# Optimization experiments

Hardware: AMD Instinct MI355X
Metric: run time of the kernel (lower is better)

## Reference

```python
import jax, jax.numpy as jnp
import numpy as np

B, N, DIM, HEADS, DEPTH, MLP = 4, 1024, 256, 4, 4, 1024
DH = DIM // HEADS
EPS = 1e-5


def _ln(x, g, b):
    mu = jnp.mean(x, axis=-1, keepdims=True)
    var = jnp.mean((x - mu) ** 2, axis=-1, keepdims=True)
    return (x - mu) / jnp.sqrt(var + EPS) * g + b


def setup_inputs() -> dict:
    key = jax.random.key(0)
    ks = jax.random.split(key, 10)
    s = 0.02
    p = {}
    p["x"] = jax.random.normal(ks[0], (B, N, DIM), jnp.float32)
    p["attn_bias"] = jax.random.normal(ks[1], (2, B, HEADS, N, N), jnp.float32)
    p["ln1_g"] = jnp.ones((DEPTH, DIM), jnp.float32)
    p["ln1_b"] = jnp.zeros((DEPTH, DIM), jnp.float32)
    p["Wkv"] = jax.random.normal(ks[2], (DEPTH, DIM, 2 * DIM), jnp.float32) * s
    p["Wq"] = jax.random.normal(ks[3], (DEPTH, DIM, DIM), jnp.float32) * s
    p["Wo"] = jax.random.normal(ks[4], (DEPTH, DIM, DIM), jnp.float32) * s
    p["bo"] = jnp.zeros((DEPTH, DIM), jnp.float32)
    p["ln2_g"] = jnp.ones((DEPTH, DIM), jnp.float32)
    p["ln2_b"] = jnp.zeros((DEPTH, DIM), jnp.float32)
    p["W1"] = jax.random.normal(ks[5], (DEPTH, DIM, MLP), jnp.float32) * s
    p["b1"] = jnp.zeros((DEPTH, MLP), jnp.float32)
    p["W2"] = jax.random.normal(ks[6], (DEPTH, MLP, DIM), jnp.float32) * s
    p["b2"] = jnp.zeros((DEPTH, DIM), jnp.float32)
    p["Wg"] = jax.random.normal(ks[7], (DIM, DIM), jnp.float32) * s
    p["lng_g"] = jnp.ones((DIM,), jnp.float32)
    p["lng_b"] = jnp.zeros((DIM,), jnp.float32)
    return p


def reference(x, attn_bias, ln1_g, ln1_b, Wkv, Wq, Wo, bo, ln2_g, ln2_b, W1, b1, W2, b2, Wg, lng_g, lng_b):
    scale = DIM ** -0.5
    add_attn = attn_bias[0] + attn_bias[1]            # [B,H,N,N]
    # aggregation bias matrices are layer-invariant (recomputed identically each layer in torch)
    A = jnp.mean(attn_bias[0], axis=1)                # [B,N,N]
    S = jnp.mean(attn_bias[1], axis=1)
    G = jax.nn.softmax(A * S, axis=2)                 # [B,N,N]

    def split_heads(t):  # [B,N,DIM] -> [B,H,N,DH]
        return t.reshape(B, N, HEADS, DH).transpose(0, 2, 1, 3)

    for l in range(DEPTH):
        # softmax-GCN aggregation
        x_ma = jax.nn.relu(_ln(jnp.matmul(G, x) @ Wg, lng_g, lng_b))
        # attention (PreNorm on x only; q comes from un-normed x_ma)
        xn = _ln(x, ln1_g[l], ln1_b[l])
        kv = xn @ Wkv[l]
        k, v = jnp.split(kv, 2, axis=-1)
        q = x_ma @ Wq[l]
        qh, kh, vh = split_heads(q), split_heads(k), split_heads(v)
        dots = jnp.einsum('bhid,bhjd->bhij', qh, kh) * scale + add_attn
        attn = jax.nn.softmax(dots, axis=-1)
        out = jnp.einsum('bhij,bhjd->bhid', attn, vh)
        out = out.transpose(0, 2, 1, 3).reshape(B, N, DIM)
        x = x + out @ Wo[l] + bo[l]
        # feed-forward (exact GELU, matching torch nn.GELU default)
        xn2 = _ln(x, ln2_g[l], ln2_b[l])
        x = x + jax.nn.gelu(xn2 @ W1[l] + b1[l], approximate=False) @ W2[l] + b2[l]
    return x
```

## Files before the change

### kernel.cpp

```cpp
#include <hip/hip_runtime.h>
#include <hip/hip_bf16.h>
#include <math.h>

typedef unsigned short u16;
typedef __bf16 bf16x8 __attribute__((ext_vector_type(8)));
typedef float f32x4 __attribute__((ext_vector_type(4)));
typedef unsigned int u32x4 __attribute__((ext_vector_type(4)));
typedef unsigned short u16x4 __attribute__((ext_vector_type(4)));

#define B_ 4
#define N_ 1024
#define DIM_ 256
#define HEADS_ 4
#define DH_ 64
#define MLP_ 1024
#define DEPTH_ 4

__device__ __forceinline__ float r2f(u16 r){ return __uint_as_float(((unsigned)r)<<16); }
__device__ __forceinline__ u16 f2r(float f){ __hip_bfloat16 h = __float2bfloat16(f); return *(u16*)&h; }

__device__ __forceinline__ float gelu_exact(float v){
  return 0.5f*v*(1.0f + erff(v*0.70710678118654752440f));
}

#define MFMA16(a,b,c) __builtin_amdgcn_mfma_f32_16x16x32_bf16(a,b,c,0,0,0)

__global__ void prep_fused(const float* __restrict__ bias, u16* __restrict__ G, u16* __restrict__ bsum,
                           const float* __restrict__ X, u16* __restrict__ Y,
                           const float* __restrict__ g, const float* __restrict__ bvec){
  if (blockIdx.x < 4096){
    int blk = blockIdx.x;
    int i = blk & (N_-1);
    int b = blk >> 10;
    int t = threadIdx.x;
    __shared__ float red[256];
    long long base0 = ((long long)(b*HEADS_)*N_ + i)*(long long)N_;
    const long long hs = (long long)N_*N_;
    const long long cs = (long long)B_*HEADS_*N_*N_;
    int j0 = t*4;
    f32x4 a = {0.f,0.f,0.f,0.f}, s = {0.f,0.f,0.f,0.f};
    #pragma unroll
    for (int h=0;h<HEADS_;h++){
      f32x4 x0 = __builtin_nontemporal_load((const f32x4*)(bias + base0 + h*hs + j0));
      f32x4 x1 = __builtin_nontemporal_load((const f32x4*)(bias + cs + base0 + h*hs + j0));
      a += x0; s += x1;
      u16x4 pk;
      #pragma unroll
      for (int k=0;k<4;k++) pk[k] = f2r(x0[k]+x1[k]);
      __builtin_nontemporal_store(pk, (u16x4*)(bsum + base0 + h*hs + j0));
    }
    float v[4]; float lmax = -3e38f;
    #pragma unroll
    for (int k=0;k<4;k++){ v[k] = (a[k]*0.25f)*(s[k]*0.25f); lmax = fmaxf(lmax, v[k]); }
    red[t]=lmax; __syncthreads();
    for (int st=128;st>0;st>>=1){ if(t<st) red[t]=fmaxf(red[t],red[t+st]); __syncthreads(); }
    float m = red[0]; __syncthreads();
    float e[4]; float lsum = 0.f;
    #pragma unroll
    for (int k=0;k<4;k++){ e[k] = __expf(v[k]-m); lsum += e[k]; }
    red[t]=lsum; __syncthreads();
    for (int st=128;st>0;st>>=1){ if(t<st) red[t]+=red[t+st]; __syncthreads(); }
    float inv = 1.0f/red[0];
    u16* Grow = G + ((long long)b*N_ + i)*(long long)N_;
    u16x4 pg;
    #pragma unroll
    for (int k=0;k<4;k++) pg[k] = f2r(e[k]*inv);
    *(u16x4*)(Grow + j0) = pg;
  } else {
    int row = (blockIdx.x-4096)*8 + (threadIdx.x>>5);
    int cg = threadIdx.x&31;
    const float* xp = X + (long long)row*DIM_ + cg*8;
    f32x4 v0 = *(const f32x4*)xp;
    f32x4 v1 = *(const f32x4*)(xp+4);
    float s = v0[0]+v0[1]+v0[2]+v0[3]+v1[0]+v1[1]+v1[2]+v1[3];
    s += __shfl_xor(s,1); s += __shfl_xor(s,2); s += __shfl_xor(s,4); s += __shfl_xor(s,8); s += __shfl_xor(s,16);
    float mu = s*(1.0f/256.0f);
    float s2 = 0.f;
    #pragma unroll
    for (int k=0;k<4;k++){ float d=v0[k]-mu; s2 += d*d; }
    #pragma unroll
    for (int k=0;k<4;k++){ float d=v1[k]-mu; s2 += d*d; }
    s2 += __shfl_xor(s2,1); s2 += __shfl_xor(s2,2); s2 += __shfl_xor(s2,4); s2 += __shfl_xor(s2,8); s2 += __shfl_xor(s2,16);
    float rstd = rsqrtf(s2*(1.0f/256.0f)+1e-5f);
    f32x4 g0 = *(const f32x4*)(g + cg*8);
    f32x4 g1 = *(const f32x4*)(g + cg*8 + 4);
    f32x4 b0 = *(const f32x4*)(bvec + cg*8);
    f32x4 b1 = *(const f32x4*)(bvec + cg*8 + 4);
    u16x4 p0, p1;
    #pragma unroll
    for (int k=0;k<4;k++) p0[k] = f2r((v0[k]-mu)*rstd*g0[k] + b0[k]);
    #pragma unroll
    for (int k=0;k<4;k++) p1[k] = f2r((v1[k]-mu)*rstd*g1[k] + b1[k]);
    u16* yp = Y + (long long)row*DIM_ + cg*8;
    *(u16x4*)yp = p0;
    *(u16x4*)(yp+4) = p1;
  }
}

__global__ void tcast_all(const float* __restrict__ Wkv, const float* __restrict__ Wq,
                          const float* __restrict__ Wo, const float* __restrict__ W1,
                          const float* __restrict__ W2, const float* __restrict__ Wg,
                          const float* __restrict__ xin,
                          u16* WkvT, u16* WqT, u16* WoT, u16* W1T, u16* W2T, u16* WgT, u16* xT){
  int z = blockIdx.z;
  const float* I; u16* O; int ldin, R, C;
  if (z < 4)       { I = Wkv + z*131072;      O = WkvT + z*131072;      ldin=512;  R=256;  C=512;  }
  else if (z < 8)  { I = Wq  + (z-4)*65536;   O = WqT  + (z-4)*65536;   ldin=256;  R=256;  C=256;  }
  else if (z < 12) { I = Wo  + (z-8)*65536;   O = WoT  + (z-8)*65536;   ldin=256;  R=256;  C=256;  }
  else if (z < 16) { I = W1  + (z-12)*262144; O = W1T  + (z-12)*262144; ldin=1024; R=256;  C=1024; }
  else if (z < 20) { I = W2  + (z-16)*262144; O = W2T  + (z-16)*262144; ldin=256;  R=1024; C=256;  }
  else if (z == 20){ I = Wg;                  O = WgT;                  ldin=256;  R=256;  C=256;  }
  else             { I = xin + (z-21)*262144; O = xT   + (z-21)*262144; ldin=256;  R=1024; C=256;  }
  int c0 = blockIdx.x*32, r0 = blockIdx.y*32;
  if (c0 >= C || r0 >= R) return;
  __shared__ float tile[32][33];
  int tx = threadIdx.x, ty = threadIdx.y;
  #pragma unroll
  for (int i=0;i<4;i++)
    tile[ty*4+i][tx] = I[(long long)(r0+ty*4+i)*ldin + c0+tx];
  __syncthreads();
  #pragma unroll
  for (int i=0;i<4;i++)
    O[(long long)(c0+ty*4+i)*R + r0+tx] = f2r(tile[tx][ty*4+i]);
}

__global__ __launch_bounds__(512, 2) void layer_pre(
    const u16* __restrict__ Gb, const u16* __restrict__ xT, const u16* __restrict__ xnb,
    const u16* __restrict__ WgT, const u16* __restrict__ WqT, const u16* __restrict__ WkvT,
    const float* __restrict__ lng, const float* __restrict__ lnb,
    u16* __restrict__ qb, u16* __restrict__ kvb, u16* __restrict__ vt)
{
  __shared__ float Gx_s[16][264];
  __shared__ float t2_s[16][264];
  __shared__ u16  xma_s[16][264];
  int tid = threadIdx.x;
  int w = tid>>6, lane = tid&63, lr = lane&15, qd = lane>>4;
  int bid = blockIdx.x;

  if (bid >= 256){
    int row0 = (bid-256)*16;
    int batch = row0>>10;
    const u16* Ap = xnb + (long long)(row0+lr)*DIM_;
    f32x4 acc[4] = {};
    for (int k0=0;k0<256;k0+=32){
      bf16x8 af = *(const bf16x8*)(Ap + k0 + qd*8);
      #pragma unroll
      for (int i=0;i<4;i++){
        bf16x8 bf = *(const bf16x8*)(WkvT + (long long)((w*4+i)*16+lr)*256 + k0 + qd*8);
        acc[i] = MFMA16(af,bf,acc[i]);
      }
    }
    #pragma unroll
    for (int i=0;i<4;i++){
      int col = (w*4+i)*16+lr;
      #pragma unroll
      for (int r=0;r<4;r++){
        int row = row0+qd*4+r;
        float v = acc[i][r];
        kvb[(long long)row*512 + col] = f2r(v);
        if (col >= 256)
          vt[(long long)batch*262144 + (long long)(col-256)*1024 + (row&1023)] = f2r(v);
      }
    }
    return;
  }

  int row0 = bid*16;
  int batch = row0>>10, brow0 = row0&1023;

  {
    int kw = w>>2, cw = w&3;
    const u16* Ap = Gb + (long long)batch*1048576 + (long long)(brow0+lr)*1024 + kw*512;
    const u16* Bp = xT + (long long)batch*262144 + (long long)kw*512;
    f32x4 acc[4] = {};
    for (int k0=0;k0<512;k0+=32){
      bf16x8 af = __builtin_nontemporal_load((const bf16x8*)(Ap + k0 + qd*8));
      #pragma unroll
      for (int nt=0;nt<4;nt++){
        bf16x8 bf = *(const bf16x8*)(Bp + (long long)(cw*64+nt*16+lr)*1024 + k0 + qd*8);
        acc[nt] = MFMA16(af,bf,acc[nt]);
      }
    }
    if (kw==0){
      #pragma unroll
      for (int nt=0;nt<4;nt++)
        #pragma unroll
        for (int r=0;r<4;r++) Gx_s[qd*4+r][cw*64+nt*16+lr] = acc[nt][r];
    }
    __syncthreads();
    if (kw==1){
      #pragma unroll
      for (int nt=0;nt<4;nt++)
        #pragma unroll
        for (int r=0;r<4;r++) Gx_s[qd*4+r][cw*64+nt*16+lr] += acc[nt][r];
    }
    __syncthreads();
  }
  {
    int r = tid>>5, cg2 = tid&31;
    #pragma unroll
    for (int i=0;i<8;i++) xma_s[r][cg2*8+i] = f2r(Gx_s[r][cg2*8+i]);
  }
  __syncthreads();
  {
    f32x4 acc[2] = {};
    for (int k0=0;k0<256;k0+=32){
      bf16x8 af = *(const bf16x8*)&xma_s[lr][k0+qd*8];
      #pragma unroll
      for (int i=0;i<2;i++){
        bf16x8 bf = *(const bf16x8*)(WgT + (long long)((w*2+i)*16+lr)*256 + k0 + qd*8);
        acc[i] = MFMA16(af,bf,acc[i]);
      }
    }
    #pragma unroll
    for (int i=0;i<2;i++)
      #pragma unroll
      for (int r=0;r<4;r++) t2_s[qd*4+r][(w*2+i)*16+lr] = acc[i][r];
  }
  __syncthreads();
  {
    int r = tid>>5, cg2 = tid&31;
    float v[8]; float s=0.f;
    #pragma unroll
    for (int i=0;i<8;i++){ v[i] = t2_s[r][cg2*8+i]; s += v[i]; }
    s += __shfl_xor(s,1); s += __shfl_xor(s,2); s += __shfl_xor(s,4); s += __shfl_xor(s,8); s += __shfl_xor(s,16);
    float mu = s*(1.0f/256.0f);
    float s2=0.f;
    #pragma unroll
    for (int i=0;i<8;i++){ float d=v[i]-mu; s2 += d*d; }
    s2 += __shfl_xor(s2,1); s2 += __shfl_xor(s2,2); s2 += __shfl_xor(s2,4); s2 += __shfl_xor(s2,8); s2 += __shfl_xor(s2,16);
    float rstd = rsqrtf(s2*(1.0f/256.0f)+1e-5f);
    #pragma unroll
    for (int i=0;i<8;i++){
      int c = cg2*8+i;
      float y = (v[i]-mu)*rstd*lng[c] + lnb[c];
      xma_s[r][c] = f2r(fmaxf(y,0.f));
    }
  }
  __syncthreads();
  {
    f32x4 acc[2] = {};
    for (int k0=0;k0<256;k0+=32){
      bf16x8 af = *(const bf16x8*)&xma_s[lr][k0+qd*8];
      #pragma unroll
      for (int i=0;i<2;i++){
        bf16x8 bf = *(const bf16x8*)(WqT + (long long)((w*2+i)*16+lr)*256 + k0 + qd*8);
        acc[i] = MFMA16(af,bf,acc[i]);
      }
    }
    #pragma unroll
    for (int i=0;i<2;i++)
      #pragma unroll
      for (int r=0;r<4;r++)
        qb[(long long)(row0+qd*4+r)*DIM_ + (w*2+i)*16+lr] = f2r(acc[i][r]);
  }
}

#define APSMEM 84224
__global__ __launch_bounds__(1024, 2) void attn_post(
    const u16* __restrict__ qb, const u16* __restrict__ kvb,
    const u16* __restrict__ vt, const u16* __restrict__ bsum,
    const float* __restrict__ resx,
    const u16* __restrict__ WoT, const float* __restrict__ bo,
    const float* __restrict__ ln2g, const float* __restrict__ ln2b,
    const u16* __restrict__ W1T, const float* __restrict__ b1,
    const u16* __restrict__ W2T, const float* __restrict__ b2,
    float* __restrict__ xf_out,
    const float* __restrict__ ln1g_next, const float* __restrict__ ln1b_next,
    u16* __restrict__ xn_out, u16* __restrict__ xT_out)
{
  __shared__ __align__(16) char smem[APSMEM];
  u16 (*sb)[16][72]   = (u16 (*)[16][72])smem;
  u16 (*Pl)[16][72]   = (u16 (*)[16][72])(smem+36864);
  float (*Ml)[16]     = (float(*)[16])(smem+73728);
  float (*Ll)[16]     = (float(*)[16])(smem+74752);
  float (*Ol)[16][68] = (float(*)[16][68])smem;
  u16  (*ao_s)[264]   = (u16 (*)[264])(smem+75776);
  float (*v_s)[264]   = (float(*)[264])smem;
  u16  (*xn2_s)[264]  = (u16 (*)[264])(smem+16896);
  u16  (*h1_s)[1048]  = (u16 (*)[1048])(smem+25344);
  float (*xnew_s)[264]= (float(*)[264])(smem+58880);

  int tid = threadIdx.x;
  int w = tid>>6, lane = tid&63, lr = lane&15, qd = lane>>4;
  int row0 = blockIdx.x*16;
  int batch = row0>>10, brow0 = row0&1023;
  int h = w>>2, g = w&3;

  f32x4 oacc[4] = {};
  float m_r[4] = {-3e38f,-3e38f,-3e38f,-3e38f};
  float l_r[4] = {0.f,0.f,0.f,0.f};
  {
    int z = batch*HEADS_ + h;
    const u16* qp = qb + ((long long)row0 + lr)*DIM_ + h*DH_;
    bf16x8 aq0 = *(const bf16x8*)(qp + qd*8);
    bf16x8 aq1 = *(const bf16x8*)(qp + 32 + qd*8);

    const u16* kbase = kvb + ((long long)(batch*N_))*512 + h*DH_;
    const u16* vbase = vt + (long long)batch*(DIM_*N_) + (long long)(h*DH_)*N_;
    const u16* bias_base = bsum + ((long long)z*N_ + brow0)*(long long)N_;
    int srr = lane>>2, scc = (lane&3)*16;

    {
      const u16* gs = bias_base + (long long)srr*N_ + (g*4)*64 + scc;
      u32x4 t0 = __builtin_nontemporal_load((const u32x4*)gs);
      u32x4 t1 = __builtin_nontemporal_load((const u32x4*)(gs+8));
      *(u32x4*)&sb[w][srr][scc]   = t0;
      *(u32x4*)&sb[w][srr][scc+8] = t1;
    }

    #pragma unroll
    for (int jtl=0; jtl<4; jtl++){
      int j0 = (g*4 + jtl)*64;
      u32x4 nb0, nb1;
      if (jtl < 3){
        const u16* gs = bias_base + (long long)srr*N_ + (j0+64) + scc;
        nb0 = __builtin_nontemporal_load((const u32x4*)gs);
        nb1 = __builtin_nontemporal_load((const u32x4*)(gs+8));
      }
      f32x4 sacc[4] = {};
      #pragma unroll
      for (int nt=0; nt<4; nt++){
        const u16* kp = kbase + (long long)(j0 + nt*16 + lr)*512;
        bf16x8 bk0 = *(const bf16x8*)(kp + qd*8);
        bf16x8 bk1 = *(const bf16x8*)(kp + 32 + qd*8);
        sacc[nt] = MFMA16(aq0, bk0, sacc[nt]);
        sacc[nt] = MFMA16(aq1, bk1, sacc[nt]);
      }
      #pragma unroll
      for (int r=0;r<4;r++){
        float pv[4];
        float vmax = -3e38f;
        #pragma unroll
        for (int nt=0;nt<4;nt++){
          float v = sacc[nt][r]*0.0625f + r2f(sb[w][qd*4+r][nt*16+lr]);
          pv[nt] = v;
          vmax = fmaxf(vmax, v);
        }
        vmax = fmaxf(vmax, __shfl_xor(vmax,1));
        vmax = fmaxf(vmax, __shfl_xor(vmax,2));
        vmax = fmaxf(vmax, __shfl_xor(vmax,4));
        vmax = fmaxf(vmax, __shfl_xor(vmax,8));
        float newm = fmaxf(m_r[r], vmax);
        float alpha = __expf(m_r[r]-newm);
        m_r[r] = newm;
        float psum = 0.f;
        #pragma unroll
        for (int nt=0;nt<4;nt++){
          float p = __expf(pv[nt]-newm);
          psum += p;
          Pl[w][qd*4+r][nt*16+lr] = f2r(p);
        }
        psum += __shfl_xor(psum,1);
        psum += __shfl_xor(psum,2);
        psum += __shfl_xor(psum,4);
        psum += __shfl_xor(psum,8);
        l_r[r] = l_r[r]*alpha + psum;
        #pragma unroll
        for (int ot=0;ot<4;ot++) oacc[ot][r] *= alpha;
      }
      if (jtl < 3){
        *(u32x4*)&sb[w][srr][scc]   = nb0;
        *(u32x4*)&sb[w][srr][scc+8] = nb1;
      }
      #pragma unroll
      for (int ks=0;ks<2;ks++){
        bf16x8 ap = *(const bf16x8*)&Pl[w][lr][ks*32 + qd*8];
        #pragma unroll
        for (int ot=0;ot<4;ot++){
          const u16* vp = vbase + (long long)(ot*16+lr)*N_ + j0 + ks*32 + qd*8;
          bf16x8 bv = *(const bf16x8*)vp;
          oacc[ot] = MFMA16(ap, bv, oacc[ot]);
        }
      }
    }
  }
  __syncthreads();
  #pragma unroll
  for (int r=0;r<4;r++){
    int row = qd*4+r;
    #pragma unroll
    for (int ot=0;ot<4;ot++) Ol[w][row][ot*16+lr] = oacc[ot][r];
    if (lr==0){ Ml[w][row] = m_r[r]; Ll[w][row] = l_r[r]; }
  }
  __syncthreads();
  if ((w&3)==0){
    #pragma unroll
    for (int r=0;r<4;r++){
      int row = qd*4+r;
      float m0 = Ml[w][row], m1 = Ml[w+1][row], m2 = Ml[w+2][row], m3 = Ml[w+3][row];
      float mm = fmaxf(fmaxf(m0,m1), fmaxf(m2,m3));
      float e0 = __expf(m0-mm), e1 = __expf(m1-mm), e2 = __expf(m2-mm), e3 = __expf(m3-mm);
      float inv = 1.0f/(Ll[w][row]*e0 + Ll[w+1][row]*e1 + Ll[w+2][row]*e2 + Ll[w+3][row]*e3);
      #pragma unroll
      for (int ot=0;ot<4;ot++){
        int c = ot*16+lr;
        float o = Ol[w][row][c]*e0 + Ol[w+1][row][c]*e1 + Ol[w+2][row][c]*e2 + Ol[w+3][row][c]*e3;
        ao_s[row][h*DH_ + c] = f2r(o*inv);
      }
    }
  }
  __syncthreads();

  {
    int kw = w>>3, cw = w&7;
    f32x4 acc[2] = {};
    for (int k0=0;k0<128;k0+=32){
      bf16x8 af = *(const bf16x8*)&ao_s[lr][kw*128 + k0 + qd*8];
      #pragma unroll
      for (int i=0;i<2;i++){
        int cv = cw*2+i;
        bf16x8 bf = *(const bf16x8*)(WoT + (long long)(cv*16+lr)*256 + kw*128 + k0 + qd*8);
        acc[i] = MFMA16(af,bf,acc[i]);
      }
    }
    if (kw==0){
      #pragma unroll
      for (int i=0;i<2;i++)
        #pragma unroll
        for (int r=0;r<4;r++) v_s[qd*4+r][(cw*2+i)*16+lr] = acc[i][r];
    }
    __syncthreads();
    if (kw==1){
      #pragma unroll
      for (int i=0;i<2;i++){
        int col = (cw*2+i)*16+lr;
        #pragma unroll
        for (int r=0;r<4;r++)
          v_s[qd*4+r][col] = v_s[qd*4+r][col] + acc[i][r] + bo[col]
                           + __builtin_nontemporal_load(&resx[(long long)(row0+qd*4+r)*DIM_ + col]);
      }
    }
    __syncthreads();
  }
  {
    int r = tid>>6, c0 = (tid&63)*4;
    float v[4]; float s=0.f;
    #pragma unroll
    for (int i=0;i<4;i++){ v[i] = v_s[r][c0+i]; s += v[i]; }
    s += __shfl_xor(s,1); s += __shfl_xor(s,2); s += __shfl_xor(s,4);
    s += __shfl_xor(s,8); s += __shfl_xor(s,16); s += __shfl_xor(s,32);
    float mu = s*(1.0f/256.0f);
    float s2=0.f;
    #pragma unroll
    for (int i=0;i<4;i++){ float d=v[i]-mu; s2 += d*d; }
    s2 += __shfl_xor(s2,1); s2 += __shfl_xor(s2,2); s2 += __shfl_xor(s2,4);
    s2 += __shfl_xor(s2,8); s2 += __shfl_xor(s2,16); s2 += __shfl_xor(s2,32);
    float rstd = rsqrtf(s2*(1.0f/256.0f)+1e-5f);
    #pragma unroll
    for (int i=0;i<4;i++){
      int c = c0+i;
      xn2_s[r][c] = f2r((v[i]-mu)*rstd*ln2g[c] + ln2b[c]);
    }
  }
  __syncthreads();
  {
    f32x4 acc[4] = {};
    for (int k0=0;k0<256;k0+=32){
      bf16x8 af = *(const bf16x8*)&xn2_s[lr][k0+qd*8];
      #pragma unroll
      for (int i=0;i<4;i++){
        int cv = w*4+i;
        bf16x8 bf = *(const bf16x8*)(W1T + (long long)(cv*16+lr)*256 + k0 + qd*8);
        acc[i] = MFMA16(af,bf,acc[i]);
      }
    }
    #pragma unroll
    for (int i=0;i<4;i++){
      int col = (w*4+i)*16+lr;
      #pragma unroll
      for (int r=0;r<4;r++)
        h1_s[qd*4+r][col] = f2r(gelu_exact(acc[i][r] + b1[col]));
    }
  }
  __syncthreads();
  {
    int kw = w>>3, cw = w&7;
    f32x4 acc[2] = {};
    for (int k0=0;k0<512;k0+=32){
      bf16x8 af = *(const bf16x8*)&h1_s[lr][kw*512 + k0 + qd*8];
      #pragma unroll
      for (int i=0;i<2;i++){
        int cv = cw*2+i;
        bf16x8 bf = *(const bf16x8*)(W2T + (long long)(cv*16+lr)*1024 + kw*512 + k0 + qd*8);
        acc[i] = MFMA16(af,bf,acc[i]);
      }
    }
    if (kw==0){
      #pragma unroll
      for (int i=0;i<2;i++)
        #pragma unroll
        for (int r=0;r<4;r++) xnew_s[qd*4+r][(cw*2+i)*16+lr] = acc[i][r];
    }
    __syncthreads();
    if (kw==1){
      #pragma unroll
      for (int i=0;i<2;i++){
        int col = (cw*2+i)*16+lr;
        #pragma unroll
        for (int r=0;r<4;r++){
          float v = xnew_s[qd*4+r][col] + acc[i][r] + b2[col] + v_s[qd*4+r][col];
          xf_out[(long long)(row0+qd*4+r)*DIM_ + col] = v;
          xnew_s[qd*4+r][col] = v;
        }
      }
    }
  }
  if (ln1g_next){
    __syncthreads();
    int r = tid>>6, c0 = (tid&63)*4;
    float v[4]; float s=0.f;
    #pragma unroll
    for (int i=0;i<4;i++){ v[i] = xnew_s[r][c0+i]; s += v[i]; }
    s += __shfl_xor(s,1); s += __shfl_xor(s,2); s += __shfl_xor(s,4);
    s += __shfl_xor(s,8); s += __shfl_xor(s,16); s += __shfl_xor(s,32);
    float mu = s*(1.0f/256.0f);
    float s2=0.f;
    #pragma unroll
    for (int i=0;i<4;i++){ float d=v[i]-mu; s2 += d*d; }
    s2 += __shfl_xor(s2,1); s2 += __shfl_xor(s2,2); s2 += __shfl_xor(s2,4);
    s2 += __shfl_xor(s2,8); s2 += __shfl_xor(s2,16); s2 += __shfl_xor(s2,32);
    float rstd = rsqrtf(s2*(1.0f/256.0f)+1e-5f);
    int grow = row0 + r;
    #pragma unroll
    for (int i=0;i<4;i++){
      int c = c0+i;
      xn_out[(long long)grow*DIM_ + c] = f2r((v[i]-mu)*rstd*ln1g_next[c] + ln1b_next[c]);
      xT_out[(long long)batch*262144 + (long long)c*1024 + (grow&1023)] = f2r(v[i]);
    }
  }
}

extern "C" void kernel_launch(void* const* d_in, const int* in_sizes, int n_in,
                              void* d_out, int out_size, void* d_ws, size_t ws_size,
                              hipStream_t stream){
  const float* x_in   = (const float*)d_in[0];
  const float* abias  = (const float*)d_in[1];
  const float* ln1_g  = (const float*)d_in[2];
  const float* ln1_b  = (const float*)d_in[3];
  const float* Wkv    = (const float*)d_in[4];
  const float* Wq     = (const float*)d_in[5];
  const float* Wo     = (const float*)d_in[6];
  const float* bo     = (const float*)d_in[7];
  const float* ln2_g  = (const float*)d_in[8];
  const float* ln2_b  = (const float*)d_in[9];
  const float* W1     = (const float*)d_in[10];
  const float* b1     = (const float*)d_in[11];
  const float* W2     = (const float*)d_in[12];
  const float* b2     = (const float*)d_in[13];
  const float* Wg     = (const float*)d_in[14];
  const float* lng_g  = (const float*)d_in[15];
  const float* lng_b  = (const float*)d_in[16];

  char* ws = (char*)d_ws;
  float* xf   = (float*)(ws);
  u16*  Gb    = (u16*)(ws + (4ll<<20));
  u16*  bsum  = (u16*)(ws + (12ll<<20));
  u16*  kvb   = (u16*)(ws + (44ll<<20));
  u16*  vt    = (u16*)(ws + (48ll<<20));
  u16*  xT    = (u16*)(ws + (50ll<<20));
  u16*  xnb   = (u16*)(ws + (52ll<<20));
  u16*  qb    = (u16*)(ws + (54ll<<20));
  u16*  WkvT  = (u16*)(ws + (58ll<<20));
  u16*  WqT   = (u16*)(ws + (59ll<<20));
  u16*  WoT   = (u16*)(ws + (59ll<<20) + (512ll<<10));
  u16*  W1T   = (u16*)(ws + (60ll<<20));
  u16*  W2T   = (u16*)(ws + (62ll<<20));
  u16*  WgT   = (u16*)(ws + (64ll<<20));

  prep_fused<<<dim3(4608), dim3(256), 0, stream>>>(abias, Gb, bsum, x_in, xnb, ln1_g, ln1_b);
  tcast_all<<<dim3(32,32,25), dim3(32,8), 0, stream>>>(Wkv,Wq,Wo,W1,W2,Wg,x_in,
                                                       WkvT,WqT,WoT,W1T,W2T,WgT,xT);

  for (int l=0; l<DEPTH_; l++){
    const float* resx = (l==0) ? x_in : xf;
    layer_pre<<<dim3(512), dim3(512), 0, stream>>>(Gb, xT, xnb,
        WgT, WqT + (long long)l*65536, WkvT + (long long)l*131072,
        lng_g, lng_b, qb, kvb, vt);
    if (l < DEPTH_-1){
      attn_post<<<dim3(256), dim3(1024), 0, stream>>>(qb, kvb, vt, bsum, resx,
          WoT + (long long)l*65536, bo + l*DIM_, ln2_g + l*DIM_, ln2_b + l*DIM_,
          W1T + (long long)l*262144, b1 + l*MLP_, W2T + (long long)l*262144, b2 + l*DIM_,
          xf, ln1_g + (l+1)*DIM_, ln1_b + (l+1)*DIM_, xnb, xT);
    } else {
      attn_post<<<dim3(256), dim3(1024), 0, stream>>>(qb, kvb, vt, bsum, resx,
          WoT + (long long)l*65536, bo + l*DIM_, ln2_g + l*DIM_, ln2_b + l*DIM_,
          W1T + (long long)l*262144, b1 + l*MLP_, W2T + (long long)l*262144, b2 + l*DIM_,
          (float*)d_out, nullptr, nullptr, nullptr, nullptr);
    }
  }
}
```

Before: 705.8 us.

## Split fused attention+MLP kernel and remap blocks for XCD-local batch/head placement

Splits the fused attention-plus-FFN kernel into a standalone flash-attention kernel and a layer_post kernel, passing the attention output through a global bf16 buffer. The attention kernel now assigns one head and 64 query rows per block, with four warps per row tile, and merges the partial softmax states in a two-step tree reduction instead of a four-way merge. Block indices in all kernels are remapped so each batch (and head pair) stays on the same pair of XCDs, improving L2 reuse of K/V and bias data. The cost is an extra kernel launch per layer and an extra global round-trip for the attention output, plus more barriers in the reduction.

```diff
diff --git a/kernel.cpp b/kernel.cpp
--- a/kernel.cpp
+++ b/kernel.cpp
@@ -136,10 +136,13 @@
   int tid = threadIdx.x;
   int w = tid>>6, lane = tid&63, lr = lane&15, qd = lane>>4;
   int bid = blockIdx.x;
+  int xcd = bid & 7, bb = xcd >> 1;
 
   if (bid >= 256){
-    int row0 = (bid-256)*16;
-    int batch = row0>>10;
+    int q = bid - 256;
+    int iblk = ((q>>3)<<1) | (xcd&1);
+    int row0 = bb*1024 + iblk*16;
+    int batch = bb;
     const u16* Ap = xnb + (long long)(row0+lr)*DIM_;
     f32x4 acc[4] = {};
     for (int k0=0;k0<256;k0+=32){
@@ -165,8 +168,9 @@
     return;
   }
 
-  int row0 = bid*16;
-  int batch = row0>>10, brow0 = row0&1023;
+  int iblk = ((bid>>3)<<1) | (xcd&1);
+  int batch = bb, brow0 = iblk*16;
+  int row0 = batch*1024 + brow0;
 
   {
     int kw = w>>2, cw = w&3;
@@ -256,49 +260,42 @@
   }
 }
 
-#define APSMEM 84224
-__global__ __launch_bounds__(1024, 2) void attn_post(
+#define FL_SMEM 73728
+__global__ __launch_bounds__(1024, 2) void flash_attn(
     const u16* __restrict__ qb, const u16* __restrict__ kvb,
     const u16* __restrict__ vt, const u16* __restrict__ bsum,
-    const float* __restrict__ resx,
-    const u16* __restrict__ WoT, const float* __restrict__ bo,
-    const float* __restrict__ ln2g, const float* __restrict__ ln2b,
-    const u16* __restrict__ W1T, const float* __restrict__ b1,
-    const u16* __restrict__ W2T, const float* __restrict__ b2,
-    float* __restrict__ xf_out,
-    const float* __restrict__ ln1g_next, const float* __restrict__ ln1b_next,
-    u16* __restrict__ xn_out, u16* __restrict__ xT_out)
+    u16* __restrict__ aob)
 {
-  __shared__ __align__(16) char smem[APSMEM];
+  __shared__ __align__(16) char smem[FL_SMEM];
   u16 (*sb)[16][72]   = (u16 (*)[16][72])smem;
   u16 (*Pl)[16][72]   = (u16 (*)[16][72])(smem+36864);
-  float (*Ml)[16]     = (float(*)[16])(smem+73728);
-  float (*Ll)[16]     = (float(*)[16])(smem+74752);
-  float (*Ol)[16][68] = (float(*)[16][68])smem;
-  u16  (*ao_s)[264]   = (u16 (*)[264])(smem+75776);
-  float (*v_s)[264]   = (float(*)[264])smem;
-  u16  (*xn2_s)[264]  = (u16 (*)[264])(smem+16896);
-  u16  (*h1_s)[1048]  = (u16 (*)[1048])(smem+25344);
-  float (*xnew_s)[264]= (float(*)[264])(smem+58880);
-
+  float (*Olb)[16][68]= (float(*)[16][68])smem;
+  float (*Mlb)[16]    = (float(*)[16])(smem+34816);
+  float (*Llb)[16]    = (float(*)[16])(smem+35328);
+
+  int p = blockIdx.x;
+  int xcd = p & 7, b = xcd >> 1;
+  int u = p >> 3;
+  int h = ((u>>4)<<1) | (xcd&1);
+  int qt = u & 15;
   int tid = threadIdx.x;
   int w = tid>>6, lane = tid&63, lr = lane&15, qd = lane>>4;
-  int row0 = blockIdx.x*16;
-  int batch = row0>>10, brow0 = row0&1023;
-  int h = w>>2, g = w&3;
+  int rt = w>>2, g = w&3;
+  int brow = qt*64 + rt*16;
+  long long grow0 = (long long)b*N_ + brow;
 
   f32x4 oacc[4] = {};
   float m_r[4] = {-3e38f,-3e38f,-3e38f,-3e38f};
   float l_r[4] = {0.f,0.f,0.f,0.f};
   {
-    int z = batch*HEADS_ + h;
-    const u16* qp = qb + ((long long)row0 + lr)*DIM_ + h*DH_;
+    int z = b*HEADS_ + h;
+    const u16* qp = qb + (grow0 + lr)*DIM_ + h*DH_;
     bf16x8 aq0 = *(const bf16x8*)(qp + qd*8);
     bf16x8 aq1 = *(const bf16x8*)(qp + 32 + qd*8);
 
-    const u16* kbase = kvb + ((long long)(batch*N_))*512 + h*DH_;
-    const u16* vbase = vt + (long long)batch*(DIM_*N_) + (long long)(h*DH_)*N_;
-    const u16* bias_base = bsum + ((long long)z*N_ + brow0)*(long long)N_;
+    const u16* kbase = kvb + ((long long)(b*N_))*512 + h*DH_;
+    const u16* vbase = vt + (long long)b*(DIM_*N_) + (long long)(h*DH_)*N_;
+    const u16* bias_base = bsum + ((long long)z*N_ + brow)*(long long)N_;
     int srr = lane>>2, scc = (lane&3)*16;
 
     {
@@ -347,9 +344,9 @@
         float psum = 0.f;
         #pragma unroll
         for (int nt=0;nt<4;nt++){
-          float p = __expf(pv[nt]-newm);
-          psum += p;
-          Pl[w][qd*4+r][nt*16+lr] = f2r(p);
+          float pp = __expf(pv[nt]-newm);
+          psum += pp;
+          Pl[w][qd*4+r][nt*16+lr] = f2r(pp);
         }
         psum += __shfl_xor(psum,1);
         psum += __shfl_xor(psum,2);
@@ -376,37 +373,87 @@
     }
   }
   __syncthreads();
-  #pragma unroll
-  for (int r=0;r<4;r++){
-    int row = qd*4+r;
-    #pragma unroll
-    for (int ot=0;ot<4;ot++) Ol[w][row][ot*16+lr] = oacc[ot][r];
-    if (lr==0){ Ml[w][row] = m_r[r]; Ll[w][row] = l_r[r]; }
-  }
-  __syncthreads();
-  if ((w&3)==0){
+  if (g & 1){
+    int slot = rt*2 + (g>>1);
     #pragma unroll
     for (int r=0;r<4;r++){
       int row = qd*4+r;
-      float m0 = Ml[w][row], m1 = Ml[w+1][row], m2 = Ml[w+2][row], m3 = Ml[w+3][row];
-      float mm = fmaxf(fmaxf(m0,m1), fmaxf(m2,m3));
-      float e0 = __expf(m0-mm), e1 = __expf(m1-mm), e2 = __expf(m2-mm), e3 = __expf(m3-mm);
-      float inv = 1.0f/(Ll[w][row]*e0 + Ll[w+1][row]*e1 + Ll[w+2][row]*e2 + Ll[w+3][row]*e3);
+      #pragma unroll
+      for (int ot=0;ot<4;ot++) Olb[slot][row][ot*16+lr] = oacc[ot][r];
+      if (lr==0){ Mlb[slot][row] = m_r[r]; Llb[slot][row] = l_r[r]; }
+    }
+  }
+  __syncthreads();
+  if (!(g & 1)){
+    int slot = rt*2 + (g>>1);
+    #pragma unroll
+    for (int r=0;r<4;r++){
+      int row = qd*4+r;
+      float m1 = Mlb[slot][row], l1 = Llb[slot][row];
+      float mm = fmaxf(m_r[r], m1);
+      float e0 = __expf(m_r[r]-mm), e1 = __expf(m1-mm);
+      m_r[r] = mm;
+      l_r[r] = l_r[r]*e0 + l1*e1;
+      #pragma unroll
+      for (int ot=0;ot<4;ot++)
+        oacc[ot][r] = oacc[ot][r]*e0 + Olb[slot][row][ot*16+lr]*e1;
+    }
+  }
+  __syncthreads();
+  if (g == 2){
+    #pragma unroll
+    for (int r=0;r<4;r++){
+      int row = qd*4+r;
+      #pragma unroll
+      for (int ot=0;ot<4;ot++) Olb[rt][row][ot*16+lr] = oacc[ot][r];
+      if (lr==0){ Mlb[rt][row] = m_r[r]; Llb[rt][row] = l_r[r]; }
+    }
+  }
+  __syncthreads();
+  if (g == 0){
+    #pragma unroll
+    for (int r=0;r<4;r++){
+      int row = qd*4+r;
+      float m1 = Mlb[rt][row], l1 = Llb[rt][row];
+      float mm = fmaxf(m_r[r], m1);
+      float e0 = __expf(m_r[r]-mm), e1 = __expf(m1-mm);
+      float linv = 1.0f/(l_r[r]*e0 + l1*e1);
       #pragma unroll
       for (int ot=0;ot<4;ot++){
-        int c = ot*16+lr;
-        float o = Ol[w][row][c]*e0 + Ol[w+1][row][c]*e1 + Ol[w+2][row][c]*e2 + Ol[w+3][row][c]*e3;
-        ao_s[row][h*DH_ + c] = f2r(o*inv);
-      }
-    }
-  }
-  __syncthreads();
+        float o = oacc[ot][r]*e0 + Olb[rt][row][ot*16+lr]*e1;
+        aob[(grow0 + row)*DIM_ + h*DH_ + ot*16 + lr] = f2r(o*linv);
+      }
+    }
+  }
+}
+
+__global__ __launch_bounds__(1024, 2) void layer_post(
+    const u16* __restrict__ aob, const float* __restrict__ resx,
+    const u16* __restrict__ WoT, const float* __restrict__ bo,
+    const float* __restrict__ ln2g, const float* __restrict__ ln2b,
+    const u16* __restrict__ W1T, const float* __restrict__ b1,
+    const u16* __restrict__ W2T, const float* __restrict__ b2,
+    float* __restrict__ xf_out,
+    const float* __restrict__ ln1g_next, const float* __restrict__ ln1b_next,
+    u16* __restrict__ xn_out, u16* __restrict__ xT_out)
+{
+  __shared__ float v_s[16][264];
+  __shared__ u16  xn2_s[16][264];
+  __shared__ u16  h1_s[16][1048];
+  __shared__ float xnew_s[16][264];
+  int tid = threadIdx.x;
+  int w = tid>>6, lane = tid&63, lr = lane&15, qd = lane>>4;
+  int p = blockIdx.x;
+  int xcd = p & 7, batch = xcd >> 1;
+  int iblk = ((p>>3)<<1) | (xcd&1);
+  int row0 = batch*1024 + iblk*16;
 
   {
     int kw = w>>3, cw = w&7;
+    const u16* Ap = aob + (long long)(row0+lr)*DIM_ + kw*128;
     f32x4 acc[2] = {};
     for (int k0=0;k0<128;k0+=32){
-      bf16x8 af = *(const bf16x8*)&ao_s[lr][kw*128 + k0 + qd*8];
+      bf16x8 af = *(const bf16x8*)(Ap + k0 + qd*8);
       #pragma unroll
       for (int i=0;i<2;i++){
         int cv = cw*2+i;
@@ -561,6 +608,7 @@
   u16*  xT    = (u16*)(ws + (50ll<<20));
   u16*  xnb   = (u16*)(ws + (52ll<<20));
   u16*  qb    = (u16*)(ws + (54ll<<20));
+  u16*  aob   = (u16*)(ws + (56ll<<20));
   u16*  WkvT  = (u16*)(ws + (58ll<<20));
   u16*  WqT   = (u16*)(ws + (59ll<<20));
   u16*  WoT   = (u16*)(ws + (59ll<<20) + (512ll<<10));
@@ -577,13 +625,14 @@
     layer_pre<<<dim3(512), dim3(512), 0, stream>>>(Gb, xT, xnb,
         WgT, WqT + (long long)l*65536, WkvT + (long long)l*131072,
         lng_g, lng_b, qb, kvb, vt);
+    flash_attn<<<dim3(256), dim3(1024), 0, stream>>>(qb, kvb, vt, bsum, aob);
     if (l < DEPTH_-1){
-      attn_post<<<dim3(256), dim3(1024), 0, stream>>>(qb, kvb, vt, bsum, resx,
+      layer_post<<<dim3(256), dim3(1024), 0, stream>>>(aob, resx,
           WoT + (long long)l*65536, bo + l*DIM_, ln2_g + l*DIM_, ln2_b + l*DIM_,
           W1T + (long long)l*262144, b1 + l*MLP_, W2T + (long long)l*262144, b2 + l*DIM_,
           xf, ln1_g + (l+1)*DIM_, ln1_b + (l+1)*DIM_, xnb, xT);
     } else {
-      attn_post<<<dim3(256), dim3(1024), 0, stream>>>(qb, kvb, vt, bsum, resx,
+      layer_post<<<dim3(256), dim3(1024), 0, stream>>>(aob, resx,
           WoT + (long long)l*65536, bo + l*DIM_, ln2_g + l*DIM_, ln2_b + l*DIM_,
           W1T + (long long)l*262144, b1 + l*MLP_, W2T + (long long)l*262144, b2 + l*DIM_,
           (float*)d_out, nullptr, nullptr, nullptr, nullptr);
```

After: 752.5 us. 6.6% more time.
